# Kernel optimization log

Measured on AMD Instinct MI355X. Metric: run time of the kernel, lower is better.

The kernel has to match this reference:

```python
import jax, jax.numpy as jnp
import numpy as np

N_NODES = 50000
N_EDGES = 800000
IN_DIM = 128
HID = 128
N_LAYERS = 3
MASK_RATE = 0.3
NUM_MASK = int(MASK_RATE * N_NODES)  # 15000


def setup_inputs() -> dict:
    key = jax.random.key(0)
    ks = jax.random.split(key, 8)
    attr = jax.random.normal(ks[0], (N_NODES, IN_DIM), dtype=jnp.float32)
    src = jax.random.randint(ks[1], (N_EDGES,), 0, N_NODES, dtype=jnp.int32)
    dst = jax.random.randint(ks[2], (N_EDGES,), 0, N_NODES, dtype=jnp.int32)
    # GraphConv weights (glorot-ish scale)
    Ws = jax.random.normal(ks[3], (N_LAYERS, HID, HID), dtype=jnp.float32) * (1.0 / np.sqrt(HID))
    bs = jnp.zeros((N_LAYERS, HID), dtype=jnp.float32)
    dec_W = jax.random.normal(ks[4], (HID, IN_DIM), dtype=jnp.float32) * (1.0 / np.sqrt(HID))
    dec_b = jnp.zeros((IN_DIM,), dtype=jnp.float32)
    mask_token = jnp.zeros((1, IN_DIM), dtype=jnp.float32)
    # torch.randperm(N)[:num_mask]
    perm = jax.random.permutation(ks[5], N_NODES)
    mask_nodes = perm[:NUM_MASK].astype(jnp.int32)
    return {"attr": attr, "src": src, "dst": dst, "Ws": Ws, "bs": bs,
            "dec_W": dec_W, "dec_b": dec_b, "mask_token": mask_token,
            "mask_nodes": mask_nodes}


def reference(attr, src, dst, Ws, bs, dec_W, dec_b, mask_token, mask_nodes):
    # degree norms (DGL GraphConv norm='both'), zero-degree clamped to 1
    ones = jnp.ones((src.shape[0],), dtype=jnp.float32)
    out_deg = jax.ops.segment_sum(ones, src, num_segments=N_NODES)
    in_deg = jax.ops.segment_sum(ones, dst, num_segments=N_NODES)
    norm_src = jnp.power(jnp.clip(out_deg, 1.0, None), -0.5)[:, None]  # [N,1]
    norm_dst = jnp.power(jnp.clip(in_deg, 1.0, None), -0.5)[:, None]

    # mask node features with the mask token
    h = attr.at[mask_nodes].set(mask_token[0])

    for i in range(N_LAYERS):
        h = h @ Ws[i]                       # [N, H]
        m = (h * norm_src)[src]             # gather: [E, H]
        agg = jax.ops.segment_sum(m, dst, num_segments=N_NODES)
        h = jax.nn.relu(agg * norm_dst + bs[i])

    recon = h @ dec_W + dec_b               # [N, IN_DIM]
    x_orig = attr[mask_nodes]
    x_rec = recon[mask_nodes]
    loss = jnp.mean((x_rec - x_orig) ** 2)
    return loss
```

## Files before the change

### kernel.cpp

```cpp
#include <hip/hip_runtime.h>
#include <hip/hip_fp16.h>

#define HID 128
#define NN 50000
#define NW4 (NN / 4)
#define NB 256
#define CST 64

typedef _Float16 f16;
typedef f16 f16x8 __attribute__((ext_vector_type(8)));
typedef float f32x4 __attribute__((ext_vector_type(4)));

__device__ __forceinline__ unsigned char enc8(float v) {
  __half h = __float2half(v);
  unsigned short b;
  __builtin_memcpy(&b, &h, 2);
  return (unsigned char)((b + 0x80u) >> 8);
}
__device__ __forceinline__ __half2 dec8lo(unsigned v) {
  unsigned p = __builtin_amdgcn_perm(0u, v, 0x01040004u);
  __half2 h2;
  __builtin_memcpy(&h2, &p, 4);
  return h2;
}
__device__ __forceinline__ __half2 dec8hi(unsigned v) {
  unsigned p = __builtin_amdgcn_perm(0u, v, 0x03040204u);
  __half2 h2;
  __builtin_memcpy(&h2, &p, 4);
  return h2;
}
__device__ __forceinline__ f16x8 dec8x8(const unsigned char* p) {
  uint2 u = *(const uint2*)p;
  unsigned r[4];
  r[0] = __builtin_amdgcn_perm(0u, u.x, 0x01040004u);
  r[1] = __builtin_amdgcn_perm(0u, u.x, 0x03040204u);
  r[2] = __builtin_amdgcn_perm(0u, u.y, 0x01040004u);
  r[3] = __builtin_amdgcn_perm(0u, u.y, 0x03040204u);
  f16x8 out;
  __builtin_memcpy(&out, r, 16);
  return out;
}
__device__ __forceinline__ __half2 xor32_add(__half2 v) {
  int b;
  __builtin_memcpy(&b, &v, 4);
  int g = __shfl_xor(b, 32);
  __half2 w;
  __builtin_memcpy(&w, &g, 4);
  return __hadd2(v, w);
}

__global__ __launch_bounds__(1024) void hist_kernel(
    const int* __restrict__ src, const int* __restrict__ dst,
    unsigned* __restrict__ pin, unsigned* __restrict__ pout,
    unsigned char* __restrict__ rank, float* __restrict__ d_out_f,
    unsigned* __restrict__ mmap_w, int E, int chunk) {
  __shared__ unsigned hist[NW4];
  const int b = blockIdx.x;
  const int e0 = b * chunk, e1 = min(E, e0 + chunk);
  if (b == 0 && threadIdx.x == 0) *d_out_f = 0.f;
  if (b < 13) {
    int wi = b * 1024 + threadIdx.x;
    if (wi < NW4) mmap_w[wi] = 0;
  }

  uint4* h4 = (uint4*)hist;
  const uint4 z4 = make_uint4(0, 0, 0, 0);
  for (int i = threadIdx.x; i < NW4 / 4; i += 1024) h4[i] = z4;
  __syncthreads();
  for (int e = e0 + threadIdx.x; e < e1; e += 1024) {
    int d = dst[e];
    unsigned sh = 8u * (d & 3);
    unsigned old = atomicAdd(&hist[d >> 2], 1u << sh);
    rank[e] = (unsigned char)((old >> sh) & 0xffu);
  }
  __syncthreads();
  uint4* rowI = (uint4*)(pin + (size_t)b * NW4);
  for (int i = threadIdx.x; i < NW4 / 4; i += 1024) {
    uint4 t = h4[i];
    rowI[i] = t;
    h4[i] = z4;
  }
  __syncthreads();
  for (int e = e0 + threadIdx.x; e < e1; e += 1024) {
    int s = src[e];
    atomicAdd(&hist[s >> 2], 1u << (8u * (s & 3)));
  }
  __syncthreads();
  uint4* rowO = (uint4*)(pout + (size_t)b * NW4);
  for (int i = threadIdx.x; i < NW4 / 4; i += 1024) rowO[i] = h4[i];
}

__global__ __launch_bounds__(1024) void merge_kernel(
    unsigned* __restrict__ pin, const unsigned* __restrict__ pout,
    int* __restrict__ in_cnt, float* __restrict__ ns,
    const int* __restrict__ mask, unsigned char* __restrict__ mmap, int nm) {
  int gi = blockIdx.x * 1024 + threadIdx.x;
  if (gi < nm) mmap[mask[gi]] = 1;

  __shared__ unsigned tsum[32][32];
  __shared__ unsigned osum[32][32];
  const int wl = threadIdx.x & 31;
  const int tile = threadIdx.x >> 5;
  const int w = blockIdx.x * 32 + wl;
  const bool ok = w < NW4;

  unsigned v[8];
  unsigned s = 0, so = 0;
  if (ok) {
#pragma unroll
    for (int j = 0; j < 8; ++j)
      v[j] = pin[(size_t)(tile * 8 + j) * NW4 + w];
#pragma unroll
    for (int j = 0; j < 8; ++j) {
      unsigned x = v[j];
      v[j] = s;
      s += x;
    }
#pragma unroll
    for (int j = 0; j < 8; ++j)
      so += pout[(size_t)(tile * 8 + j) * NW4 + w];
  }
  tsum[tile][wl] = s;
  osum[tile][wl] = so;
  __syncthreads();
  unsigned toff = 0;
  for (int k = 0; k < tile; ++k) toff += tsum[k][wl];
  if (ok) {
#pragma unroll
    for (int j = 0; j < 8; ++j)
      pin[(size_t)(tile * 8 + j) * NW4 + w] = v[j] + toff;
    if (tile == 31) {
      unsigned tin = toff + s;
      unsigned tout = 0;
#pragma unroll
      for (int k = 0; k < 32; ++k) tout += osum[k][wl];
      int i0 = tin & 0xffu, i1 = (tin >> 8) & 0xffu,
          i2 = (tin >> 16) & 0xffu, i3 = (tin >> 24) & 0xffu;
      int o0 = tout & 0xffu, o1 = (tout >> 8) & 0xffu,
          o2 = (tout >> 16) & 0xffu, o3 = (tout >> 24) & 0xffu;
      ((int4*)in_cnt)[w] = make_int4(i0, i1, i2, i3);
      ((float4*)ns)[w] = make_float4(rsqrtf((float)max(o0, 1)),
                                     rsqrtf((float)max(o1, 1)),
                                     rsqrtf((float)max(o2, 1)),
                                     rsqrtf((float)max(o3, 1)));
    }
  }
}

__global__ __launch_bounds__(256) void fillprep_kernel(
    const int* __restrict__ src, const int* __restrict__ dst,
    const unsigned char* __restrict__ rank, const unsigned* __restrict__ pin,
    int* __restrict__ csr,
    const float* __restrict__ attr, const float* __restrict__ Ws,
    const float* __restrict__ decW, const float* __restrict__ ns,
    const float* __restrict__ token, const unsigned char* __restrict__ mmap,
    unsigned char* __restrict__ X, f16* __restrict__ Wt,
    int E, int chunk, int n4) {
  const int b = blockIdx.x;
  if (b < 1024) {
    const int c = b >> 2;
    const int cs = c * chunk;
    const int ce = min(E, cs + chunk);
    const int len = ce - cs;
    const int q = b & 3;
    const int qe0 = cs + (len * q) / 4;
    const int qe1 = cs + (len * (q + 1)) / 4;
    const unsigned* __restrict__ row = pin + (size_t)c * NW4;
    for (int e = qe0 + threadIdx.x; e < qe1; e += 256) {
      int s = src[e], d = dst[e];
      unsigned base = (row[d >> 2] >> (8u * (d & 3))) & 0xffu;
      csr[d * CST + (int)base + (int)rank[e]] = s;
    }
  } else if (b < 1280) {
    int i = (b - 1024) * 256 + threadIdx.x;
    int m = i >> 14, rem = i & 16383, n = rem >> 7, k = rem & 127;
    const float* Wsrc = (m < 3) ? (Ws + (size_t)m * 16384) : decW;
    Wt[i] = (f16)Wsrc[k * 128 + n];
  } else {
    int i = (b - 1280) * 256 + threadIdx.x;
    if (i < n4) {
      int r = i >> 5, c4 = i & 31;
      float s = ns[r];
      float4 v = mmap[r] ? ((const float4*)token)[c4] : ((const float4*)attr)[i];
      ((uchar4*)X)[i] = make_uchar4(enc8(s * v.x), enc8(s * v.y),
                                    enc8(s * v.z), enc8(s * v.w));
    }
  }
}

__global__ __launch_bounds__(256) void agg_kernel(
    const unsigned* __restrict__ Xw, const int* __restrict__ csr,
    const int* __restrict__ in_cnt, const int* __restrict__ glist,
    unsigned* __restrict__ Y, int n) {
  int ni = (blockIdx.x * blockDim.x + threadIdx.x) >> 6;
  int lane = threadIdx.x & 63;
  if (ni >= n) return;
  int node = glist ? glist[ni] : ni;
  int cnt = in_cnt[node];
  int idx = csr[node * CST + lane];
  const int half = lane >> 5, sub = lane & 31;
  const __half2 z = __floats2half2_rn(0.f, 0.f);
  __half2 a00 = z, a01 = z, a10 = z, a11 = z;
  __half2 a20 = z, a21 = z, a30 = z, a31 = z;
  int i = 0;
  for (; i + 8 <= cnt; i += 8) {
    int s0 = __shfl(idx, i + 0 + half);
    int s1 = __shfl(idx, i + 2 + half);
    int s2 = __shfl(idx, i + 4 + half);
    int s3 = __shfl(idx, i + 6 + half);
    unsigned u0 = Xw[(size_t)s0 * 32 + sub];
    unsigned u1 = Xw[(size_t)s1 * 32 + sub];
    unsigned u2 = Xw[(size_t)s2 * 32 + sub];
    unsigned u3 = Xw[(size_t)s3 * 32 + sub];
    a00 = __hadd2(a00, dec8lo(u0));
    a01 = __hadd2(a01, dec8hi(u0));
    a10 = __hadd2(a10, dec8lo(u1));
    a11 = __hadd2(a11, dec8hi(u1));
    a20 = __hadd2(a20, dec8lo(u2));
    a21 = __hadd2(a21, dec8hi(u2));
    a30 = __hadd2(a30, dec8lo(u3));
    a31 = __hadd2(a31, dec8hi(u3));
  }
  for (; i + 2 <= cnt; i += 2) {
    int s = __shfl(idx, i + half);
    unsigned u = Xw[(size_t)s * 32 + sub];
    a00 = __hadd2(a00, dec8lo(u));
    a01 = __hadd2(a01, dec8hi(u));
  }
  if (i < cnt) {
    int s = __shfl(idx, i);
    unsigned u = Xw[(size_t)s * 32 + sub];
    if (half) u = 0;
    a00 = __hadd2(a00, dec8lo(u));
    a01 = __hadd2(a01, dec8hi(u));
  }
  __half2 s0 = __hadd2(__hadd2(a00, a10), __hadd2(a20, a30));
  __half2 s1 = __hadd2(__hadd2(a01, a11), __hadd2(a21, a31));
  s0 = xor32_add(s0);
  s1 = xor32_add(s1);
  float ndv = rsqrtf((float)max(cnt, 1));
  float2 f0 = __half22float2(s0);
  float2 f1 = __half22float2(s1);
  if (half == 0) {
    unsigned pack = (unsigned)enc8(f0.x * ndv) |
                    ((unsigned)enc8(f0.y * ndv) << 8) |
                    ((unsigned)enc8(f1.x * ndv) << 16) |
                    ((unsigned)enc8(f1.y * ndv) << 24);
    Y[(size_t)ni * 32 + sub] = pack;
  }
}

__global__ __launch_bounds__(256) void gemm_layer_kernel(
    const unsigned char* __restrict__ A8, const f16* __restrict__ Wt,
    unsigned char* __restrict__ out, const float* __restrict__ col_bias,
    const float* __restrict__ row_scale, int M) {
  __shared__ f16 Bs[128 * 136];
  const int t = threadIdx.x;
  for (int i = t; i < 2048; i += 256) {
    int n = i >> 4, c = i & 15;
    *(f16x8*)&Bs[n * 136 + c * 8] = *(const f16x8*)&Wt[n * 128 + c * 8];
  }
  const int wave = t >> 6, lane = t & 63;
  const int ln = lane & 15, kq = lane >> 4;
  const int mBase = blockIdx.x * 64 + wave * 16;

  const int am = mBase + ln;
  const int rowA = (am < M) ? am : 0;
  const unsigned char* Ap = A8 + (size_t)rowA * HID + kq * 8;
  f16x8 af[4];
#pragma unroll
  for (int ki = 0; ki < 4; ++ki) af[ki] = dec8x8(Ap + ki * 32);

  f32x4 acc[8];
#pragma unroll
  for (int nt = 0; nt < 8; ++nt) acc[nt] = (f32x4){0.f, 0.f, 0.f, 0.f};
  __syncthreads();
#pragma unroll
  for (int ki = 0; ki < 4; ++ki) {
#pragma unroll
    for (int nt = 0; nt < 8; ++nt) {
      f16x8 bf = *(const f16x8*)&Bs[(nt * 16 + ln) * 136 + ki * 32 + kq * 8];
      acc[nt] = __builtin_amdgcn_mfma_f32_16x16x32_f16(af[ki], bf, acc[nt], 0, 0, 0);
    }
  }
  const int orow = mBase + kq * 4;
  float rs[4];
#pragma unroll
  for (int r = 0; r < 4; ++r)
    rs[r] = (row_scale && orow + r < M) ? row_scale[orow + r] : 1.f;
#pragma unroll
  for (int nt = 0; nt < 8; ++nt) {
    int col = nt * 16 + ln;
    float bb = col_bias[col];
#pragma unroll
    for (int r = 0; r < 4; ++r) {
      int gr = orow + r;
      if (gr < M) {
        float v = fmaxf(acc[nt][r] + bb, 0.f) * rs[r];
        out[(size_t)gr * HID + col] = enc8(v);
      }
    }
  }
}

__global__ __launch_bounds__(256) void gemm2_loss_kernel(
    const unsigned char* __restrict__ A8, const f16* __restrict__ W2t,
    const f16* __restrict__ Dt, const float* __restrict__ b2,
    const float* __restrict__ decb, const int* __restrict__ mask,
    const float* __restrict__ attr, float* __restrict__ out,
    int M, float scale) {
  __shared__ f16 Bs[128 * 136];
  __shared__ f16 Ds[128 * 136];
  __shared__ f16 Ar[64 * 136];
  const int t = threadIdx.x;
  for (int i = t; i < 2048; i += 256) {
    int n = i >> 4, c = i & 15;
    *(f16x8*)&Bs[n * 136 + c * 8] = *(const f16x8*)&W2t[n * 128 + c * 8];
    *(f16x8*)&Ds[n * 136 + c * 8] = *(const f16x8*)&Dt[n * 128 + c * 8];
  }
  const int wave = t >> 6, lane = t & 63;
  const int ln = lane & 15, kq = lane >> 4;
  const int mBase = blockIdx.x * 64 + wave * 16;

  const int am = mBase + ln;
  const int rowA = (am < M) ? am : 0;
  const unsigned char* Ap = A8 + (size_t)rowA * HID + kq * 8;
  f16x8 af[4];
#pragma unroll
  for (int ki = 0; ki < 4; ++ki) af[ki] = dec8x8(Ap + ki * 32);

  f32x4 acc[8];
#pragma unroll
  for (int nt = 0; nt < 8; ++nt) acc[nt] = (f32x4){0.f, 0.f, 0.f, 0.f};
  __syncthreads();
#pragma unroll
  for (int ki = 0; ki < 4; ++ki) {
#pragma unroll
    for (int nt = 0; nt < 8; ++nt) {
      f16x8 bf = *(const f16x8*)&Bs[(nt * 16 + ln) * 136 + ki * 32 + kq * 8];
      acc[nt] = __builtin_amdgcn_mfma_f32_16x16x32_f16(af[ki], bf, acc[nt], 0, 0, 0);
    }
  }
  const int orow = mBase + kq * 4;
#pragma unroll
  for (int nt = 0; nt < 8; ++nt) {
    int col = nt * 16 + ln;
    float bb = b2[col];
#pragma unroll
    for (int r = 0; r < 4; ++r) {
      float v = fmaxf(acc[nt][r] + bb, 0.f);
      Ar[(wave * 16 + kq * 4 + r) * 136 + col] = (f16)v;
    }
  }
  __syncthreads();

#pragma unroll
  for (int ki = 0; ki < 4; ++ki)
    af[ki] = *(const f16x8*)&Ar[(wave * 16 + ln) * 136 + ki * 32 + kq * 8];
#pragma unroll
  for (int nt = 0; nt < 8; ++nt) acc[nt] = (f32x4){0.f, 0.f, 0.f, 0.f};
#pragma unroll
  for (int ki = 0; ki < 4; ++ki) {
#pragma unroll
    for (int nt = 0; nt < 8; ++nt) {
      f16x8 bf = *(const f16x8*)&Ds[(nt * 16 + ln) * 136 + ki * 32 + kq * 8];
      acc[nt] = __builtin_amdgcn_mfma_f32_16x16x32_f16(af[ki], bf, acc[nt], 0, 0, 0);
    }
  }
  int mrow[4];
#pragma unroll
  for (int r = 0; r < 4; ++r) mrow[r] = (orow + r < M) ? mask[orow + r] : -1;
  float part = 0.f;
#pragma unroll
  for (int nt = 0; nt < 8; ++nt) {
    int col = nt * 16 + ln;
    float bb = decb[col];
#pragma unroll
    for (int r = 0; r < 4; ++r) {
      if (mrow[r] >= 0) {
        float d = acc[nt][r] + bb - attr[(size_t)mrow[r] * HID + col];
        part += d * d;
      }
    }
  }
#pragma unroll
  for (int off = 32; off > 0; off >>= 1) part += __shfl_down(part, off);
  __shared__ float wsum[4];
  if (lane == 0) wsum[wave] = part;
  __syncthreads();
  if (t == 0)
    atomicAdd(out, (wsum[0] + wsum[1] + wsum[2] + wsum[3]) * scale);
}

extern "C" void kernel_launch(void* const* d_in, const int* in_sizes, int n_in,
                              void* d_out, int out_size, void* d_ws, size_t ws_size,
                              hipStream_t stream) {
  const float* attr  = (const float*)d_in[0];
  const int*   src   = (const int*)d_in[1];
  const int*   dst   = (const int*)d_in[2];
  const float* Ws    = (const float*)d_in[3];
  const float* bs    = (const float*)d_in[4];
  const float* decW  = (const float*)d_in[5];
  const float* decb  = (const float*)d_in[6];
  const float* token = (const float*)d_in[7];
  const int*   mask  = (const int*)d_in[8];

  const int N  = in_sizes[0] / HID;
  const int E  = in_sizes[1];
  const int NM = in_sizes[8];
  const int chunk = (E + NB - 1) / NB;

  char* w = (char*)d_ws;
  unsigned char* X = (unsigned char*)w;  w += (size_t)N * HID;
  unsigned char* Y = (unsigned char*)w;  w += (size_t)N * HID;
  f16* Wt = (f16*)w;           w += (size_t)4 * HID * HID * 2;
  int* csr = (int*)w;          w += (size_t)NN * CST * 4;
  unsigned char* rank = (unsigned char*)w;  w += (size_t)E;
  unsigned* pin = (unsigned*)w;  w += (size_t)NB * NW4 * 4;
  unsigned* pout = (unsigned*)w; w += (size_t)NB * NW4 * 4;
  int* in_cnt = (int*)w;       w += (size_t)N * 4;
  float* ns = (float*)w;       w += (size_t)N * 4;
  unsigned char* mmap = (unsigned char*)w;  w += (size_t)NW4 * 4;

  hist_kernel<<<NB, 1024, 0, stream>>>(src, dst, pin, pout, rank,
                                       (float*)d_out, (unsigned*)mmap, E, chunk);
  merge_kernel<<<(NW4 + 31) / 32, 1024, 0, stream>>>(pin, pout, in_cnt, ns,
                                                     mask, mmap, NM);

  int prep_blocks = 1280 + (N * 32 + 255) / 256;
  fillprep_kernel<<<prep_blocks, 256, 0, stream>>>(
      src, dst, rank, pin, csr, attr, Ws, decW, ns, token, mmap,
      X, Wt, E, chunk, N * 32);

  for (int l = 0; l < 2; ++l) {
    agg_kernel<<<(N + 3) / 4, 256, 0, stream>>>(
        (const unsigned*)X, csr, in_cnt, nullptr, (unsigned*)Y, N);
    gemm_layer_kernel<<<(N + 63) / 64, 256, 0, stream>>>(
        Y, Wt + (size_t)l * HID * HID, X, bs + (size_t)l * HID, ns, N);
  }

  agg_kernel<<<(NM + 3) / 4, 256, 0, stream>>>(
      (const unsigned*)X, csr, in_cnt, mask, (unsigned*)Y, NM);

  gemm2_loss_kernel<<<(NM + 63) / 64, 256, 0, stream>>>(
      Y, Wt + (size_t)2 * HID * HID, Wt + (size_t)3 * HID * HID,
      bs + 2 * HID, decb, mask, attr, (float*)d_out,
      NM, 1.f / ((float)NM * HID));
}
```

Measured before the change: 218.8 us.

## Fuse neighbor aggregation with per-layer GEMM in one 1024-thread kernel

Merges the gather/aggregate kernel and the following GEMM into one kernel per layer, and does the same for the last aggregation plus the GEMM-and-loss tail. A 1024-thread block aggregates 16 nodes, one wave each, stages the rows in shared memory as fp16, then 8 waves run the 16x128x128 MFMA. This removes the 8-bit intermediate Y round trip through global memory and cuts the number of launches. In exchange each block reloads the full 128x128 weight tile for only 16 rows, half the waves sit idle during the GEMM, and the large block may lower occupancy.

New measurement: 215.1 us. No clear change (-1.7%).

```diff
diff --git a/kernel.cpp b/kernel.cpp
--- a/kernel.cpp
+++ b/kernel.cpp
@@ -28,17 +28,6 @@
   __half2 h2;
   __builtin_memcpy(&h2, &p, 4);
   return h2;
-}
-__device__ __forceinline__ f16x8 dec8x8(const unsigned char* p) {
-  uint2 u = *(const uint2*)p;
-  unsigned r[4];
-  r[0] = __builtin_amdgcn_perm(0u, u.x, 0x01040004u);
-  r[1] = __builtin_amdgcn_perm(0u, u.x, 0x03040204u);
-  r[2] = __builtin_amdgcn_perm(0u, u.y, 0x01040004u);
-  r[3] = __builtin_amdgcn_perm(0u, u.y, 0x03040204u);
-  f16x8 out;
-  __builtin_memcpy(&out, r, 16);
-  return out;
 }
 __device__ __forceinline__ __half2 xor32_add(__half2 v) {
   int b;
@@ -188,15 +177,9 @@
   }
 }
 
-__global__ __launch_bounds__(256) void agg_kernel(
+__device__ __forceinline__ void gather_sums(
     const unsigned* __restrict__ Xw, const int* __restrict__ csr,
-    const int* __restrict__ in_cnt, const int* __restrict__ glist,
-    unsigned* __restrict__ Y, int n) {
-  int ni = (blockIdx.x * blockDim.x + threadIdx.x) >> 6;
-  int lane = threadIdx.x & 63;
-  if (ni >= n) return;
-  int node = glist ? glist[ni] : ni;
-  int cnt = in_cnt[node];
+    int node, int cnt, int lane, __half2& o0, __half2& o1) {
   int idx = csr[node * CST + lane];
   const int half = lane >> 5, sub = lane & 31;
   const __half2 z = __floats2half2_rn(0.f, 0.f);
@@ -236,160 +219,152 @@
   }
   __half2 s0 = __hadd2(__hadd2(a00, a10), __hadd2(a20, a30));
   __half2 s1 = __hadd2(__hadd2(a01, a11), __hadd2(a21, a31));
-  s0 = xor32_add(s0);
-  s1 = xor32_add(s1);
-  float ndv = rsqrtf((float)max(cnt, 1));
-  float2 f0 = __half22float2(s0);
-  float2 f1 = __half22float2(s1);
-  if (half == 0) {
-    unsigned pack = (unsigned)enc8(f0.x * ndv) |
-                    ((unsigned)enc8(f0.y * ndv) << 8) |
-                    ((unsigned)enc8(f1.x * ndv) << 16) |
-                    ((unsigned)enc8(f1.y * ndv) << 24);
-    Y[(size_t)ni * 32 + sub] = pack;
-  }
-}
-
-__global__ __launch_bounds__(256) void gemm_layer_kernel(
-    const unsigned char* __restrict__ A8, const f16* __restrict__ Wt,
-    unsigned char* __restrict__ out, const float* __restrict__ col_bias,
-    const float* __restrict__ row_scale, int M) {
+  o0 = xor32_add(s0);
+  o1 = xor32_add(s1);
+}
+
+__global__ __launch_bounds__(1024) void layer_kernel(
+    const unsigned* __restrict__ Xw, const int* __restrict__ csr,
+    const int* __restrict__ in_cnt, const f16* __restrict__ Wt,
+    const float* __restrict__ col_bias, const float* __restrict__ row_scale,
+    unsigned char* __restrict__ Xout, int M) {
   __shared__ f16 Bs[128 * 136];
+  __shared__ f16 Ar[16 * 136];
   const int t = threadIdx.x;
-  for (int i = t; i < 2048; i += 256) {
+  for (int i = t; i < 2048; i += 1024) {
     int n = i >> 4, c = i & 15;
     *(f16x8*)&Bs[n * 136 + c * 8] = *(const f16x8*)&Wt[n * 128 + c * 8];
   }
   const int wave = t >> 6, lane = t & 63;
-  const int ln = lane & 15, kq = lane >> 4;
-  const int mBase = blockIdx.x * 64 + wave * 16;
-
-  const int am = mBase + ln;
-  const int rowA = (am < M) ? am : 0;
-  const unsigned char* Ap = A8 + (size_t)rowA * HID + kq * 8;
-  f16x8 af[4];
-#pragma unroll
-  for (int ki = 0; ki < 4; ++ki) af[ki] = dec8x8(Ap + ki * 32);
-
-  f32x4 acc[8];
-#pragma unroll
-  for (int nt = 0; nt < 8; ++nt) acc[nt] = (f32x4){0.f, 0.f, 0.f, 0.f};
-  __syncthreads();
-#pragma unroll
-  for (int ki = 0; ki < 4; ++ki) {
-#pragma unroll
-    for (int nt = 0; nt < 8; ++nt) {
-      f16x8 bf = *(const f16x8*)&Bs[(nt * 16 + ln) * 136 + ki * 32 + kq * 8];
-      acc[nt] = __builtin_amdgcn_mfma_f32_16x16x32_f16(af[ki], bf, acc[nt], 0, 0, 0);
-    }
-  }
-  const int orow = mBase + kq * 4;
-  float rs[4];
-#pragma unroll
-  for (int r = 0; r < 4; ++r)
-    rs[r] = (row_scale && orow + r < M) ? row_scale[orow + r] : 1.f;
-#pragma unroll
-  for (int nt = 0; nt < 8; ++nt) {
-    int col = nt * 16 + ln;
-    float bb = col_bias[col];
+  const int node = blockIdx.x * 16 + wave;
+
+  __half2 s0 = __floats2half2_rn(0.f, 0.f), s1 = s0;
+  int cnt = 0;
+  if (node < M) {
+    cnt = in_cnt[node];
+    gather_sums(Xw, csr, node, cnt, lane, s0, s1);
+  }
+  if ((lane >> 5) == 0) {
+    float ndv = rsqrtf((float)max(cnt, 1));
+    float2 f0 = __half22float2(s0);
+    float2 f1 = __half22float2(s1);
+    int sub = lane & 31;
+    *(__half2*)&Ar[wave * 136 + 4 * sub] = __floats2half2_rn(f0.x * ndv, f0.y * ndv);
+    *(__half2*)&Ar[wave * 136 + 4 * sub + 2] = __floats2half2_rn(f1.x * ndv, f1.y * ndv);
+  }
+  __syncthreads();
+
+  if (wave < 8) {
+    const int ln = lane & 15, kq = lane >> 4;
+    f32x4 acc = (f32x4){0.f, 0.f, 0.f, 0.f};
+#pragma unroll
+    for (int ki = 0; ki < 4; ++ki) {
+      f16x8 af = *(const f16x8*)&Ar[ln * 136 + ki * 32 + kq * 8];
+      f16x8 bf = *(const f16x8*)&Bs[(wave * 16 + ln) * 136 + ki * 32 + kq * 8];
+      acc = __builtin_amdgcn_mfma_f32_16x16x32_f16(af, bf, acc, 0, 0, 0);
+    }
+    const int orow = blockIdx.x * 16 + kq * 4;
+    const int col = wave * 16 + ln;
+    const float bb = col_bias[col];
 #pragma unroll
     for (int r = 0; r < 4; ++r) {
       int gr = orow + r;
       if (gr < M) {
-        float v = fmaxf(acc[nt][r] + bb, 0.f) * rs[r];
-        out[(size_t)gr * HID + col] = enc8(v);
+        float rs = row_scale ? row_scale[gr] : 1.f;
+        float v = fmaxf(acc[r] + bb, 0.f) * rs;
+        Xout[(size_t)gr * HID + col] = enc8(v);
       }
     }
   }
 }
 
-__global__ __launch_bounds__(256) void gemm2_loss_kernel(
-    const unsigned char* __restrict__ A8, const f16* __restrict__ W2t,
+__global__ __launch_bounds__(1024) void tail_kernel(
+    const unsigned* __restrict__ Xw, const int* __restrict__ csr,
+    const int* __restrict__ in_cnt, const f16* __restrict__ W2t,
     const f16* __restrict__ Dt, const float* __restrict__ b2,
     const float* __restrict__ decb, const int* __restrict__ mask,
     const float* __restrict__ attr, float* __restrict__ out,
     int M, float scale) {
   __shared__ f16 Bs[128 * 136];
   __shared__ f16 Ds[128 * 136];
-  __shared__ f16 Ar[64 * 136];
+  __shared__ f16 Ar[16 * 136];
+  __shared__ f16 Ar2[16 * 136];
   const int t = threadIdx.x;
-  for (int i = t; i < 2048; i += 256) {
+  for (int i = t; i < 2048; i += 1024) {
     int n = i >> 4, c = i & 15;
     *(f16x8*)&Bs[n * 136 + c * 8] = *(const f16x8*)&W2t[n * 128 + c * 8];
     *(f16x8*)&Ds[n * 136 + c * 8] = *(const f16x8*)&Dt[n * 128 + c * 8];
   }
   const int wave = t >> 6, lane = t & 63;
+  const int ni = blockIdx.x * 16 + wave;
+
+  __half2 s0 = __floats2half2_rn(0.f, 0.f), s1 = s0;
+  int cnt = 0;
+  if (ni < M) {
+    int node = mask[ni];
+    cnt = in_cnt[node];
+    gather_sums(Xw, csr, node, cnt, lane, s0, s1);
+  }
+  if ((lane >> 5) == 0) {
+    float ndv = rsqrtf((float)max(cnt, 1));
+    float2 f0 = __half22float2(s0);
+    float2 f1 = __half22float2(s1);
+    int sub = lane & 31;
+    *(__half2*)&Ar[wave * 136 + 4 * sub] = __floats2half2_rn(f0.x * ndv, f0.y * ndv);
+    *(__half2*)&Ar[wave * 136 + 4 * sub + 2] = __floats2half2_rn(f1.x * ndv, f1.y * ndv);
+  }
+  __syncthreads();
+
   const int ln = lane & 15, kq = lane >> 4;
-  const int mBase = blockIdx.x * 64 + wave * 16;
-
-  const int am = mBase + ln;
-  const int rowA = (am < M) ? am : 0;
-  const unsigned char* Ap = A8 + (size_t)rowA * HID + kq * 8;
-  f16x8 af[4];
-#pragma unroll
-  for (int ki = 0; ki < 4; ++ki) af[ki] = dec8x8(Ap + ki * 32);
-
-  f32x4 acc[8];
-#pragma unroll
-  for (int nt = 0; nt < 8; ++nt) acc[nt] = (f32x4){0.f, 0.f, 0.f, 0.f};
-  __syncthreads();
-#pragma unroll
-  for (int ki = 0; ki < 4; ++ki) {
-#pragma unroll
-    for (int nt = 0; nt < 8; ++nt) {
-      f16x8 bf = *(const f16x8*)&Bs[(nt * 16 + ln) * 136 + ki * 32 + kq * 8];
-      acc[nt] = __builtin_amdgcn_mfma_f32_16x16x32_f16(af[ki], bf, acc[nt], 0, 0, 0);
-    }
-  }
-  const int orow = mBase + kq * 4;
-#pragma unroll
-  for (int nt = 0; nt < 8; ++nt) {
-    int col = nt * 16 + ln;
-    float bb = b2[col];
+  if (wave < 8) {
+    f32x4 acc = (f32x4){0.f, 0.f, 0.f, 0.f};
+#pragma unroll
+    for (int ki = 0; ki < 4; ++ki) {
+      f16x8 af = *(const f16x8*)&Ar[ln * 136 + ki * 32 + kq * 8];
+      f16x8 bf = *(const f16x8*)&Bs[(wave * 16 + ln) * 136 + ki * 32 + kq * 8];
+      acc = __builtin_amdgcn_mfma_f32_16x16x32_f16(af, bf, acc, 0, 0, 0);
+    }
+    const int col = wave * 16 + ln;
+    const float bb = b2[col];
+#pragma unroll
+    for (int r = 0; r < 4; ++r)
+      Ar2[(kq * 4 + r) * 136 + col] = (f16)fmaxf(acc[r] + bb, 0.f);
+  }
+  __syncthreads();
+
+  float part = 0.f;
+  if (wave < 8) {
+    f32x4 acc = (f32x4){0.f, 0.f, 0.f, 0.f};
+#pragma unroll
+    for (int ki = 0; ki < 4; ++ki) {
+      f16x8 af = *(const f16x8*)&Ar2[ln * 136 + ki * 32 + kq * 8];
+      f16x8 bf = *(const f16x8*)&Ds[(wave * 16 + ln) * 136 + ki * 32 + kq * 8];
+      acc = __builtin_amdgcn_mfma_f32_16x16x32_f16(af, bf, acc, 0, 0, 0);
+    }
+    const int col = wave * 16 + ln;
+    const float bb = decb[col];
+    const int orow = blockIdx.x * 16 + kq * 4;
 #pragma unroll
     for (int r = 0; r < 4; ++r) {
-      float v = fmaxf(acc[nt][r] + bb, 0.f);
-      Ar[(wave * 16 + kq * 4 + r) * 136 + col] = (f16)v;
-    }
-  }
-  __syncthreads();
-
-#pragma unroll
-  for (int ki = 0; ki < 4; ++ki)
-    af[ki] = *(const f16x8*)&Ar[(wave * 16 + ln) * 136 + ki * 32 + kq * 8];
-#pragma unroll
-  for (int nt = 0; nt < 8; ++nt) acc[nt] = (f32x4){0.f, 0.f, 0.f, 0.f};
-#pragma unroll
-  for (int ki = 0; ki < 4; ++ki) {
-#pragma unroll
-    for (int nt = 0; nt < 8; ++nt) {
-      f16x8 bf = *(const f16x8*)&Ds[(nt * 16 + ln) * 136 + ki * 32 + kq * 8];
-      acc[nt] = __builtin_amdgcn_mfma_f32_16x16x32_f16(af[ki], bf, acc[nt], 0, 0, 0);
-    }
-  }
-  int mrow[4];
-#pragma unroll
-  for (int r = 0; r < 4; ++r) mrow[r] = (orow + r < M) ? mask[orow + r] : -1;
-  float part = 0.f;
-#pragma unroll
-  for (int nt = 0; nt < 8; ++nt) {
-    int col = nt * 16 + ln;
-    float bb = decb[col];
-#pragma unroll
-    for (int r = 0; r < 4; ++r) {
-      if (mrow[r] >= 0) {
-        float d = acc[nt][r] + bb - attr[(size_t)mrow[r] * HID + col];
+      int gni = orow + r;
+      if (gni < M) {
+        int node = mask[gni];
+        float d = acc[r] + bb - attr[(size_t)node * HID + col];
         part += d * d;
       }
     }
-  }
-#pragma unroll
-  for (int off = 32; off > 0; off >>= 1) part += __shfl_down(part, off);
-  __shared__ float wsum[4];
-  if (lane == 0) wsum[wave] = part;
-  __syncthreads();
-  if (t == 0)
-    atomicAdd(out, (wsum[0] + wsum[1] + wsum[2] + wsum[3]) * scale);
+#pragma unroll
+    for (int off = 32; off > 0; off >>= 1) part += __shfl_down(part, off);
+  }
+  __shared__ float wsum[8];
+  if (wave < 8 && lane == 0) wsum[wave] = part;
+  __syncthreads();
+  if (t == 0) {
+    float tot = 0.f;
+#pragma unroll
+    for (int k = 0; k < 8; ++k) tot += wsum[k];
+    atomicAdd(out, tot * scale);
+  }
 }
 
 extern "C" void kernel_launch(void* const* d_in, const int* in_sizes, int n_in,
@@ -432,18 +407,15 @@
       src, dst, rank, pin, csr, attr, Ws, decW, ns, token, mmap,
       X, Wt, E, chunk, N * 32);
 
-  for (int l = 0; l < 2; ++l) {
-    agg_kernel<<<(N + 3) / 4, 256, 0, stream>>>(
-        (const unsigned*)X, csr, in_cnt, nullptr, (unsigned*)Y, N);
-    gemm_layer_kernel<<<(N + 63) / 64, 256, 0, stream>>>(
-        Y, Wt + (size_t)l * HID * HID, X, bs + (size_t)l * HID, ns, N);
-  }
-
-  agg_kernel<<<(NM + 3) / 4, 256, 0, stream>>>(
-      (const unsigned*)X, csr, in_cnt, mask, (unsigned*)Y, NM);
-
-  gemm2_loss_kernel<<<(NM + 63) / 64, 256, 0, stream>>>(
-      Y, Wt + (size_t)2 * HID * HID, Wt + (size_t)3 * HID * HID,
+  layer_kernel<<<(N + 15) / 16, 1024, 0, stream>>>(
+      (const unsigned*)X, csr, in_cnt, Wt, bs, ns, Y, N);
+  layer_kernel<<<(N + 15) / 16, 1024, 0, stream>>>(
+      (const unsigned*)Y, csr, in_cnt, Wt + (size_t)HID * HID,
+      bs + HID, ns, X, N);
+
+  tail_kernel<<<(NM + 15) / 16, 1024, 0, stream>>>(
+      (const unsigned*)X, csr, in_cnt,
+      Wt + (size_t)2 * HID * HID, Wt + (size_t)3 * HID * HID,
       bs + 2 * HID, decb, mask, attr, (float*)d_out,
       NM, 1.f / ((float)NM * HID));
 }
```
